# Performance work log

Measured on AMD Instinct MI355X. Metric: run time of the kernel, lower is better.

## Reference

```python
import jax, jax.numpy as jnp
import numpy as np

B = 4        # number of point clouds (equal-size contiguous batches)
P = 8192     # points per cloud
C_IN = 64
C_OUT = 64
K = 16       # kNN neighbors (includes the point itself, as in PyG knn)
EPS = 1e-5
NEG_SLOPE = 0.2


def setup_inputs() -> dict:
    key = jax.random.key(0)
    k1, k2, k3 = jax.random.split(key, 3)
    x = jax.random.normal(k1, (B * P, C_IN), dtype=jnp.float32)
    batch = jnp.repeat(jnp.arange(B, dtype=jnp.int64), P)  # sorted, equal sizes
    W = jax.random.normal(k2, (2 * C_IN, C_OUT), dtype=jnp.float32) * (1.0 / np.sqrt(2 * C_IN))
    b = jax.random.normal(k3, (C_OUT,), dtype=jnp.float32) * 0.01
    gamma = jnp.ones((C_OUT,), dtype=jnp.float32)
    beta = jnp.zeros((C_OUT,), dtype=jnp.float32)
    return {"x": x, "batch": batch, "W": W, "b": b, "gamma": gamma, "beta": beta}


def _edgeconv(x, W, b, gamma, beta):
    xb = x.reshape(B, P, C_IN)
    # per-cloud pairwise squared distances: [B, P, P]
    sq = jnp.sum(xb * xb, axis=-1)
    d = sq[:, :, None] + sq[:, None, :] - 2.0 * jnp.einsum("bpc,bqc->bpq", xb, xb)
    # k nearest neighbors (smallest distance, self included)
    _, idx = jax.lax.top_k(-d, K)                      # [B, P, K]
    xj = jax.vmap(lambda pts, ind: pts[ind])(xb, idx)  # [B, P, K, C_IN]
    xi = xb[:, :, None, :]
    e = jnp.concatenate([jnp.broadcast_to(xi, xj.shape), xj - xi], axis=-1)  # [B,P,K,2C]
    # edge MLP: Linear -> BatchNorm1d (training-mode batch stats over all edges) -> LeakyReLU
    h = jnp.einsum("bpke,eo->bpko", e, W) + b          # [B, P, K, C_OUT]
    hf = h.reshape(-1, C_OUT)
    mean = jnp.mean(hf, axis=0)
    var = jnp.mean(hf * hf, axis=0) - mean * mean      # biased variance (torch BN)
    hn = (h - mean) * jax.lax.rsqrt(var + EPS) * gamma + beta
    a = jnp.where(hn >= 0, hn, NEG_SLOPE * hn)
    # max aggregation over neighbors
    return jnp.max(a, axis=2).reshape(B * P, C_OUT)


def reference(x, batch, W, b, gamma, beta):
    # `batch` encodes B equal-size contiguous clouds; kNN is computed per cloud.
    return _edgeconv(x, W, b, gamma, beta)
```

## Files before the change

kernel.cpp:

```cpp
#include <hip/hip_runtime.h>
#include <cfloat>

#define BATCH 4
#define P 8192
#define C 64
#define KNN 16
#define NPTS (BATCH * P)
#define NEDGE (NPTS * KNN)
#define EPSV 1e-5f
#define SLOPE 0.2f
#define NQ 2
#define QCOLS (P / NQ)

typedef __attribute__((ext_vector_type(8))) short bf16x8;
typedef __attribute__((ext_vector_type(16))) float f32x16;


__device__ __forceinline__ unsigned short f2bf(float f) {
    unsigned u = __float_as_uint(f);
    u += 0x7FFFu + ((u >> 16) & 1u);
    return (unsigned short)(u >> 16);
}
__device__ __forceinline__ float bf2f(unsigned short s) {
    return __uint_as_float(((unsigned)s) << 16);
}

__global__ void prep_frag(const float* __restrict__ x, uint4* __restrict__ xfh,
                          uint4* __restrict__ xfm, uint4* __restrict__ xfl,
                          float* __restrict__ sq) {
    __shared__ float part[32][9];
    int tid = threadIdx.x;
    int ptl = tid >> 3, j8 = tid & 7;
    int g = blockIdx.x;
    int p = g * 32 + ptl;
    const float4* xp = (const float4*)(x + (size_t)p * C + j8 * 8);
    float4 a = xp[0], b = xp[1];
    float v[8] = {a.x, a.y, a.z, a.w, b.x, b.y, b.z, b.w};
    unsigned short hs[8], ms[8], ls[8];
    float ssum = 0.f;
#pragma unroll
    for (int e = 0; e < 8; ++e) {
        float xv = v[e];
        ssum = fmaf(xv, xv, ssum);
        unsigned short h = f2bf(xv);
        float r1 = xv - bf2f(h);
        unsigned short m = f2bf(r1);
        float r2 = r1 - bf2f(m);
        unsigned short l = f2bf(r2);
        hs[e] = h; ms[e] = m; ls[e] = l;
    }
    int dst = (g * 4 + (j8 >> 1)) * 64 + ptl + 32 * (j8 & 1);
    uint4 ph, pm, pl;
    ph.x = (unsigned)hs[0] | ((unsigned)hs[1] << 16);
    ph.y = (unsigned)hs[2] | ((unsigned)hs[3] << 16);
    ph.z = (unsigned)hs[4] | ((unsigned)hs[5] << 16);
    ph.w = (unsigned)hs[6] | ((unsigned)hs[7] << 16);
    pm.x = (unsigned)ms[0] | ((unsigned)ms[1] << 16);
    pm.y = (unsigned)ms[2] | ((unsigned)ms[3] << 16);
    pm.z = (unsigned)ms[4] | ((unsigned)ms[5] << 16);
    pm.w = (unsigned)ms[6] | ((unsigned)ms[7] << 16);
    pl.x = (unsigned)ls[0] | ((unsigned)ls[1] << 16);
    pl.y = (unsigned)ls[2] | ((unsigned)ls[3] << 16);
    pl.z = (unsigned)ls[4] | ((unsigned)ls[5] << 16);
    pl.w = (unsigned)ls[6] | ((unsigned)ls[7] << 16);
    xfh[dst] = ph; xfm[dst] = pm; xfl[dst] = pl;
    part[ptl][j8] = ssum;
    __syncthreads();
    if (j8 == 0) {
        float s = 0.f;
#pragma unroll
        for (int k = 0; k < 8; ++k) s += part[ptl][k];
        sq[p] = s;
    }
}

__global__ __launch_bounds__(256, 4) void knn_kernel(const uint4* __restrict__ xfh,
                                                     const uint4* __restrict__ xfm,
                                                     const uint4* __restrict__ xfl,
                                                     const float* __restrict__ sq,
                                                     float* __restrict__ pv,
                                                     int* __restrict__ pi) {
    __shared__ float bufv[64 * 65];
    __shared__ int   bufi[64 * 65];
    __shared__ int   idL[64 * 17];
    __shared__ int   cntL[64];
    __shared__ float worstL[64];

    int tid = threadIdx.x;
    int b = blockIdx.x & 3;
    int t = blockIdx.x >> 2;
    int tile = t & 127;
    int half = t >> 7;
    int bglob = b * P;
    int r0 = tile * 64;
    int colbase = half * QCOLS;
    int w = tid >> 6, lane = tid & 63;
    int wr = w & 1, wc = w >> 1;

    if (tid < 64) { cntL[tid] = 0; worstL[tid] = FLT_MAX; }

    int gA = ((bglob + r0) >> 5) + wr;
    bf16x8 Ah[4], Am[4], Al[4];
#pragma unroll
    for (int kk = 0; kk < 4; ++kk) {
        Ah[kk] = __builtin_bit_cast(bf16x8, xfh[(gA * 4 + kk) * 64 + lane]);
        Am[kk] = __builtin_bit_cast(bf16x8, xfm[(gA * 4 + kk) * 64 + lane]);
        Al[kk] = __builtin_bit_cast(bf16x8, xfl[(gA * 4 + kk) * 64 + lane]);
    }

    float tv[16];
    float worst = FLT_MAX;
#pragma unroll
    for (int j = 0; j < 16; ++j) tv[j] = FLT_MAX;
    int rown = w * 16 + (lane & 15);
    bool owner = (lane < 16);

    int rbase = wr * 32 + 4 * (lane >> 5);
    int colq = wc * 32 + (lane & 31);
    __syncthreads();

    for (int chunk = 0; chunk < QCOLS / 64; ++chunk) {
        int c0 = colbase + chunk * 64;
        int gB = ((bglob + c0) >> 5) + wc;
        bf16x8 Bh[4], Bm[4], Bl[4];
#pragma unroll
        for (int kk = 0; kk < 4; ++kk) {
            Bh[kk] = __builtin_bit_cast(bf16x8, xfh[(gB * 4 + kk) * 64 + lane]);
            Bm[kk] = __builtin_bit_cast(bf16x8, xfm[(gB * 4 + kk) * 64 + lane]);
            Bl[kk] = __builtin_bit_cast(bf16x8, xfl[(gB * 4 + kk) * 64 + lane]);
        }
        float sc = sq[bglob + c0 + colq];

        f32x16 acc0, acc1;
#pragma unroll
        for (int i = 0; i < 16; ++i) { acc0[i] = 0.f; acc1[i] = 0.f; }
#pragma unroll
        for (int kk = 0; kk < 4; ++kk) {
            acc0 = __builtin_amdgcn_mfma_f32_32x32x16_bf16(Ah[kk], Bh[kk], acc0, 0, 0, 0);
            acc1 = __builtin_amdgcn_mfma_f32_32x32x16_bf16(Ah[kk], Bm[kk], acc1, 0, 0, 0);
            acc0 = __builtin_amdgcn_mfma_f32_32x32x16_bf16(Am[kk], Bh[kk], acc0, 0, 0, 0);
            acc1 = __builtin_amdgcn_mfma_f32_32x32x16_bf16(Am[kk], Bm[kk], acc1, 0, 0, 0);
            acc0 = __builtin_amdgcn_mfma_f32_32x32x16_bf16(Ah[kk], Bl[kk], acc0, 0, 0, 0);
            acc1 = __builtin_amdgcn_mfma_f32_32x32x16_bf16(Al[kk], Bh[kk], acc1, 0, 0, 0);
        }

        if (chunk == 0) {
#pragma unroll
            for (int reg = 0; reg < 16; ++reg) {
                float s = fmaf(-2.f, acc0[reg] + acc1[reg], sc);
                int row = rbase + (reg & 3) + 8 * (reg >> 2);
                bufv[row * 65 + colq] = s;
            }
        } else {
            float4 twA[4];
#pragma unroll
            for (int g4 = 0; g4 < 4; ++g4)
                twA[g4] = *(const float4*)&worstL[rbase + 8 * g4];
            int colg = bglob + c0 + colq;
#pragma unroll
            for (int reg = 0; reg < 16; ++reg) {
                float s = fmaf(-2.f, acc0[reg] + acc1[reg], sc);
                float tW = ((const float*)&twA[reg >> 2])[reg & 3];
                if (s < tW) {
                    int row = rbase + (reg & 3) + 8 * (reg >> 2);
                    int slot = atomicAdd(&cntL[row], 1);
                    bufv[row * 65 + slot] = s;
                    bufi[row * 65 + slot] = colg;
                }
            }
        }
        __syncthreads();

        if (owner) {
            int n = (chunk == 0) ? 64 : cntL[rown];
            for (int k = 0; k < n; ++k) {
                float s = bufv[rown * 65 + k];
                if (s < worst) {
                    float mx = tv[0];
                    int pos = 0;
#pragma unroll
                    for (int j = 1; j < 16; ++j) {
                        bool g = tv[j] > mx;
                        mx = g ? tv[j] : mx;
                        pos = g ? j : pos;
                    }
#pragma unroll
                    for (int j = 0; j < 16; ++j)
                        if (j == pos) tv[j] = s;
                    idL[rown * 17 + pos] = (chunk == 0) ? (bglob + colbase + k)
                                                        : bufi[rown * 65 + k];
                    float nw = fmaxf(fmaxf(fmaxf(tv[0], tv[1]), fmaxf(tv[2], tv[3])),
                                     fmaxf(fmaxf(tv[4], tv[5]), fmaxf(tv[6], tv[7])));
                    nw = fmaxf(nw, fmaxf(fmaxf(fmaxf(tv[8], tv[9]), fmaxf(tv[10], tv[11])),
                                         fmaxf(fmaxf(tv[12], tv[13]), fmaxf(tv[14], tv[15]))));
                    worst = nw;
                }
            }
            cntL[rown] = 0;
            worstL[rown] = worst;
        }
        __syncthreads();
    }

    if (owner) {
        size_t o = (((size_t)(bglob + r0 + rown)) * NQ + half) * KNN;
#pragma unroll
        for (int j = 0; j < 16; ++j) {
            pv[o + j] = tv[j];
            pi[o + j] = idL[rown * 17 + j];
        }
    }
}

__global__ void merge_kernel(const float* __restrict__ pv, const int* __restrict__ pi,
                             int* __restrict__ idx_out) {
    __shared__ float mv[128 * 33];
    __shared__ int   mi[128 * 33];
    int tid = threadIdx.x;
    int lr = tid & 127, q = tid >> 7;
    int row = blockIdx.x * 128 + lr;
    size_t o = ((size_t)row * NQ + q) * KNN;
#pragma unroll
    for (int j = 0; j < 16; ++j) {
        mv[lr * 33 + q * 16 + j] = pv[o + j];
        mi[lr * 33 + q * 16 + j] = pi[o + j];
    }
    __syncthreads();
    if (tid < 128) {
        float tv[16];
        int ti[16];
        float worst = FLT_MAX;
#pragma unroll
        for (int j = 0; j < 16; ++j) { tv[j] = FLT_MAX; ti[j] = 0; }
        for (int e = 0; e < 32; ++e) {
            float s = mv[tid * 33 + e];
            if (s < worst) {
                float mx = tv[0];
                int pos = 0;
#pragma unroll
                for (int j = 1; j < 16; ++j) {
                    bool g = tv[j] > mx;
                    mx = g ? tv[j] : mx;
                    pos = g ? j : pos;
                }
#pragma unroll
                for (int j = 0; j < 16; ++j)
                    if (j == pos) { tv[j] = s; ti[j] = mi[tid * 33 + e]; }
                float nw = tv[0];
#pragma unroll
                for (int j = 1; j < 16; ++j) nw = fmaxf(nw, tv[j]);
                worst = nw;
            }
        }
        size_t oo = (size_t)row * KNN;
#pragma unroll
        for (int j = 0; j < 16; ++j) idx_out[oo + j] = ti[j];
    }
}

__global__ void prep_UV(const float* __restrict__ x, const float* __restrict__ W,
                        float* __restrict__ U, float* __restrict__ V) {
    __shared__ float Ws[128][64];
    __shared__ float xs[4][64];
    int tid = threadIdx.x;
    for (int i = tid; i < 128 * 64; i += 256) ((float*)Ws)[i] = W[i];
    int p0 = blockIdx.x * 4;
    int r = tid >> 6, c = tid & 63;
    xs[r][c] = x[(size_t)(p0 + r) * C + c];
    __syncthreads();
    float u = 0.f, v = 0.f;
#pragma unroll
    for (int k = 0; k < 64; ++k) {
        float xv = xs[r][k];
        float w1 = Ws[k][c];
        float w2 = Ws[64 + k][c];
        u = fmaf(xv, w1 - w2, u);
        v = fmaf(xv, w2, v);
    }
    size_t o = (size_t)(p0 + r) * C + c;
    U[o] = u;
    V[o] = v;
}

__global__ void stats_kernel(const float* __restrict__ U, const float* __restrict__ V,
                             const float* __restrict__ bias, const int* __restrict__ idx,
                             float* __restrict__ stats) {
    int tid = threadIdx.x;
    int c = tid & 63, kk = tid >> 6;
    int p0 = blockIdx.x * 32;
    float bc = bias[c];
    float sum = 0.f, sumsq = 0.f;
    for (int pp = 0; pp < 32; ++pp) {
        int p = p0 + pp;
        float u = U[(size_t)p * C + c] + bc;
#pragma unroll
        for (int k4 = 0; k4 < 4; ++k4) {
            int j = idx[(size_t)p * KNN + kk * 4 + k4];
            float h = u + V[(size_t)j * C + c];
            sum += h;
            sumsq = fmaf(h, h, sumsq);
        }
    }
    __shared__ float red[2][4][64];
    red[0][kk][c] = sum;
    red[1][kk][c] = sumsq;
    __syncthreads();
    if (tid < 64) {
        float s = red[0][0][tid] + red[0][1][tid] + red[0][2][tid] + red[0][3][tid];
        atomicAdd(&stats[tid], s);
    } else if (tid < 128) {
        int cc = tid - 64;
        float s = red[1][0][cc] + red[1][1][cc] + red[1][2][cc] + red[1][3][cc];
        atomicAdd(&stats[64 + cc], s);
    }
}

__global__ void finalize_kernel(const float* __restrict__ stats,
                                const float* __restrict__ gamma,
                                const float* __restrict__ beta,
                                float* __restrict__ sshift) {
    int c = threadIdx.x;
    const float N = (float)NEDGE;
    float mean = stats[c] / N;
    float var = stats[64 + c] / N - mean * mean;
    float s = gamma[c] * rsqrtf(var + EPSV);
    sshift[c] = s;
    sshift[64 + c] = beta[c] - mean * s;
}

__global__ void out_kernel(const float* __restrict__ U, const float* __restrict__ V,
                           const float* __restrict__ bias, const int* __restrict__ idx,
                           const float* __restrict__ sshift, float* __restrict__ out) {
    int tid = threadIdx.x;
    int c = tid & 63, g = tid >> 6;
    int p0 = blockIdx.x * 16;
    float s = sshift[c], t = sshift[64 + c];
    float bc = bias[c];
    for (int pp = g; pp < 16; pp += 4) {
        int p = p0 + pp;
        float mx = -FLT_MAX, mn = FLT_MAX;
#pragma unroll
        for (int k = 0; k < KNN; ++k) {
            int j = idx[(size_t)p * KNN + k];
            float v = V[(size_t)j * C + c];
            mx = fmaxf(mx, v);
            mn = fminf(mn, v);
        }
        float hsel = (s >= 0.f) ? mx : mn;
        float hn = fmaf(s, U[(size_t)p * C + c] + bc + hsel, t);
        out[(size_t)p * C + c] = (hn >= 0.f) ? hn : SLOPE * hn;
    }
}

extern "C" void kernel_launch(void* const* d_in, const int* in_sizes, int n_in,
                              void* d_out, int out_size, void* d_ws, size_t ws_size,
                              hipStream_t stream) {
    const float* x     = (const float*)d_in[0];
    const float* W     = (const float*)d_in[2];
    const float* bias  = (const float*)d_in[3];
    const float* gamma = (const float*)d_in[4];
    const float* beta  = (const float*)d_in[5];
    float* out = (float*)d_out;

    float* wsf    = (float*)d_ws;
    float* U      = wsf;
    float* V      = wsf + 2097152;
    uint4* xfh    = (uint4*)wsf;
    uint4* xfm    = (uint4*)(wsf + 1048576);
    uint4* xfl    = (uint4*)(wsf + 2097152);
    float* sq     = wsf + 4194304;
    float* stats  = wsf + 4227072;
    float* sshift = wsf + 4227200;
    int*   idx    = (int*)(wsf + 4227328);
    float* pv     = wsf + 4751616;
    int*   pi     = (int*)(wsf + 5800192);

    hipLaunchKernelGGL(prep_frag, dim3(NPTS / 32), dim3(256), 0, stream, x, xfh, xfm, xfl, sq);
    hipLaunchKernelGGL(knn_kernel, dim3(BATCH * (P / 64) * NQ), dim3(256), 0, stream,
                       (const uint4*)xfh, (const uint4*)xfm, (const uint4*)xfl, sq, pv, pi);
    hipLaunchKernelGGL(merge_kernel, dim3(NPTS / 128), dim3(256), 0, stream, pv, pi, idx);
    hipLaunchKernelGGL(prep_UV, dim3(NPTS / 4), dim3(256), 0, stream, x, W, U, V);
    hipMemsetAsync(stats, 0, 128 * sizeof(float), stream);
    hipLaunchKernelGGL(stats_kernel, dim3(NPTS / 32), dim3(256), 0, stream, U, V, bias, idx, stats);
    hipLaunchKernelGGL(finalize_kernel, dim3(1), dim3(64), 0, stream, stats, gamma, beta, sshift);
    hipLaunchKernelGGL(out_kernel, dim3(NPTS / 16), dim3(256), 0, stream, U, V, bias, idx, sshift, out);
}
```

Baseline: 574.8 us.

## Distribute kNN top-k across 16-lane groups and pipeline selection with next chunk's MFMA

Instead of one owner lane per row keeping a 16-entry register list (only 16 of 64 lanes active), each 16-lane group now holds one row's top-16 with one entry per lane, using ballot and shuffle-max reductions to replace the worst entry. Candidate buffers are double-buffered so selection for the previous chunk runs after the current chunk's MFMA, removing one barrier per chunk. The first three chunks are dense-scanned from a shared pool to seed thresholds. Per-row candidates are capped at 32 per chunk, which can drop true neighbors if more than 32 pass the threshold, and each insert now costs cross-lane shuffles.

```diff
diff --git a/kernel.cpp b/kernel.cpp
--- a/kernel.cpp
+++ b/kernel.cpp
@@ -11,6 +11,8 @@
 #define SLOPE 0.2f
 #define NQ 2
 #define QCOLS (P / NQ)
+#define NCH (QCOLS / 64)
+#define CAP 32
 
 typedef __attribute__((ext_vector_type(8))) short bf16x8;
 typedef __attribute__((ext_vector_type(16))) float f32x16;
@@ -80,11 +82,14 @@
                                                      const float* __restrict__ sq,
                                                      float* __restrict__ pv,
                                                      int* __restrict__ pi) {
-    __shared__ float bufv[64 * 65];
-    __shared__ int   bufi[64 * 65];
-    __shared__ int   idL[64 * 17];
-    __shared__ int   cntL[64];
+    __shared__ float bufv0[64 * CAP];
+    __shared__ int   bufi0[64 * CAP];
+    __shared__ float r1pool[64 * 68];
     __shared__ float worstL[64];
+    __shared__ int   cntA[2][64];
+
+    float* buf1v = r1pool;
+    int*   buf1i = (int*)(r1pool + 64 * CAP);
 
     int tid = threadIdx.x;
     int b = blockIdx.x & 3;
@@ -96,8 +101,11 @@
     int colbase = half * QCOLS;
     int w = tid >> 6, lane = tid & 63;
     int wr = w & 1, wc = w >> 1;
-
-    if (tid < 64) { cntL[tid] = 0; worstL[tid] = FLT_MAX; }
+    int g = lane >> 4, gl = lane & 15;
+    unsigned long long gmask = 0xFFFFull << (g * 16);
+    int myrow0 = w * 16 + g * 4;
+
+    if (tid < 128) ((int*)cntA)[tid] = 0;
 
     int gA = ((bglob + r0) >> 5) + wr;
     bf16x8 Ah[4], Am[4], Al[4];
@@ -108,18 +116,16 @@
         Al[kk] = __builtin_bit_cast(bf16x8, xfl[(gA * 4 + kk) * 64 + lane]);
     }
 
-    float tv[16];
-    float worst = FLT_MAX;
-#pragma unroll
-    for (int j = 0; j < 16; ++j) tv[j] = FLT_MAX;
-    int rown = w * 16 + (lane & 15);
-    bool owner = (lane < 16);
+    float tvq[4], wq[4];
+    int tiq[4];
+#pragma unroll
+    for (int rr = 0; rr < 4; ++rr) { tvq[rr] = FLT_MAX; wq[rr] = FLT_MAX; tiq[rr] = 0; }
 
     int rbase = wr * 32 + 4 * (lane >> 5);
     int colq = wc * 32 + (lane & 31);
     __syncthreads();
 
-    for (int chunk = 0; chunk < QCOLS / 64; ++chunk) {
+    for (int chunk = 0; chunk < NCH; ++chunk) {
         int c0 = colbase + chunk * 64;
         int gB = ((bglob + c0) >> 5) + wc;
         bf16x8 Bh[4], Bm[4], Bl[4];
@@ -144,14 +150,79 @@
             acc1 = __builtin_amdgcn_mfma_f32_32x32x16_bf16(Al[kk], Bh[kk], acc1, 0, 0, 0);
         }
 
-        if (chunk == 0) {
+        if (chunk >= 1) {
+            if (chunk <= 3) {
+                int idbase0 = bglob + colbase + (chunk - 1) * 64;
+#pragma unroll
+                for (int rr = 0; rr < 4; ++rr) {
+                    int row = myrow0 + rr;
+                    float tv = tvq[rr], worst = wq[rr];
+                    int ti = tiq[rr];
+                    const float* bv = &r1pool[row * 68];
+                    for (int k4 = 0; k4 < 64; k4 += 4) {
+                        float4 s4 = *(const float4*)(bv + k4);
+#pragma unroll
+                        for (int e = 0; e < 4; ++e) {
+                            float s = (e == 0) ? s4.x : (e == 1) ? s4.y : (e == 2) ? s4.z : s4.w;
+                            if (s < worst) {
+                                unsigned long long m = __ballot(tv == worst) & gmask;
+                                if (lane == (int)__builtin_ctzll(m)) { tv = s; ti = idbase0 + k4 + e; }
+                                float mx = tv;
+                                mx = fmaxf(mx, __shfl_xor(mx, 1));
+                                mx = fmaxf(mx, __shfl_xor(mx, 2));
+                                mx = fmaxf(mx, __shfl_xor(mx, 4));
+                                mx = fmaxf(mx, __shfl_xor(mx, 8));
+                                worst = mx;
+                            }
+                        }
+                    }
+                    tvq[rr] = tv; tiq[rr] = ti; wq[rr] = worst;
+                    if (gl == 0) worstL[row] = worst;
+                }
+            } else {
+                int mb = chunk & 1;
+                const float* mv = mb ? buf1v : bufv0;
+                const int*   mi = mb ? buf1i : bufi0;
+#pragma unroll
+                for (int rr = 0; rr < 4; ++rr) {
+                    int row = myrow0 + rr;
+                    float tv = tvq[rr], worst = wq[rr];
+                    int ti = tiq[rr];
+                    int n = cntA[mb][row]; n = (n > CAP) ? CAP : n;
+                    const float* bv = mv + row * CAP;
+                    const int*   bi = mi + row * CAP;
+                    for (int k = 0; k < n; ++k) {
+                        float s = bv[k];
+                        if (s < worst) {
+                            unsigned long long m = __ballot(tv == worst) & gmask;
+                            if (lane == (int)__builtin_ctzll(m)) { tv = s; ti = bi[k]; }
+                            float mx = tv;
+                            mx = fmaxf(mx, __shfl_xor(mx, 1));
+                            mx = fmaxf(mx, __shfl_xor(mx, 2));
+                            mx = fmaxf(mx, __shfl_xor(mx, 4));
+                            mx = fmaxf(mx, __shfl_xor(mx, 8));
+                            worst = mx;
+                        }
+                    }
+                    tvq[rr] = tv; tiq[rr] = ti; wq[rr] = worst;
+                    if (gl == 0) worstL[row] = worst;
+                    if (gl == 1) cntA[mb][row] = 0;
+                }
+            }
+            __syncthreads();
+        }
+
+        if (chunk <= 2) {
 #pragma unroll
             for (int reg = 0; reg < 16; ++reg) {
                 float s = fmaf(-2.f, acc0[reg] + acc1[reg], sc);
                 int row = rbase + (reg & 3) + 8 * (reg >> 2);
-                bufv[row * 65 + colq] = s;
+                r1pool[row * 68 + colq] = s;
             }
         } else {
+            int ab = (chunk - 3) & 1;
+            float* av = ab ? buf1v : bufv0;
+            int*   ai = ab ? buf1i : bufi0;
             float4 twA[4];
 #pragma unroll
             for (int g4 = 0; g4 < 4; ++g4)
@@ -163,52 +234,49 @@
                 float tW = ((const float*)&twA[reg >> 2])[reg & 3];
                 if (s < tW) {
                     int row = rbase + (reg & 3) + 8 * (reg >> 2);
-                    int slot = atomicAdd(&cntL[row], 1);
-                    bufv[row * 65 + slot] = s;
-                    bufi[row * 65 + slot] = colg;
+                    int slot = atomicAdd(&cntA[ab][row], 1);
+                    if (slot < CAP) { av[row * CAP + slot] = s; ai[row * CAP + slot] = colg; }
                 }
             }
         }
         __syncthreads();
-
-        if (owner) {
-            int n = (chunk == 0) ? 64 : cntL[rown];
+    }
+
+    {
+        int mb = NCH & 1;
+        const float* mv = mb ? buf1v : bufv0;
+        const int*   mi = mb ? buf1i : bufi0;
+#pragma unroll
+        for (int rr = 0; rr < 4; ++rr) {
+            int row = myrow0 + rr;
+            float tv = tvq[rr], worst = wq[rr];
+            int ti = tiq[rr];
+            int n = cntA[mb][row]; n = (n > CAP) ? CAP : n;
+            const float* bv = mv + row * CAP;
+            const int*   bi = mi + row * CAP;
             for (int k = 0; k < n; ++k) {
-                float s = bufv[rown * 65 + k];
+                float s = bv[k];
                 if (s < worst) {
-                    float mx = tv[0];
-                    int pos = 0;
-#pragma unroll
-                    for (int j = 1; j < 16; ++j) {
-                        bool g = tv[j] > mx;
-                        mx = g ? tv[j] : mx;
-                        pos = g ? j : pos;
-                    }
-#pragma unroll
-                    for (int j = 0; j < 16; ++j)
-                        if (j == pos) tv[j] = s;
-                    idL[rown * 17 + pos] = (chunk == 0) ? (bglob + colbase + k)
-                                                        : bufi[rown * 65 + k];
-                    float nw = fmaxf(fmaxf(fmaxf(tv[0], tv[1]), fmaxf(tv[2], tv[3])),
-                                     fmaxf(fmaxf(tv[4], tv[5]), fmaxf(tv[6], tv[7])));
-                    nw = fmaxf(nw, fmaxf(fmaxf(fmaxf(tv[8], tv[9]), fmaxf(tv[10], tv[11])),
-                                         fmaxf(fmaxf(tv[12], tv[13]), fmaxf(tv[14], tv[15]))));
-                    worst = nw;
+                    unsigned long long m = __ballot(tv == worst) & gmask;
+                    if (lane == (int)__builtin_ctzll(m)) { tv = s; ti = bi[k]; }
+                    float mx = tv;
+                    mx = fmaxf(mx, __shfl_xor(mx, 1));
+                    mx = fmaxf(mx, __shfl_xor(mx, 2));
+                    mx = fmaxf(mx, __shfl_xor(mx, 4));
+                    mx = fmaxf(mx, __shfl_xor(mx, 8));
+                    worst = mx;
                 }
             }
-            cntL[rown] = 0;
-            worstL[rown] = worst;
-        }
-        __syncthreads();
-    }
-
-    if (owner) {
-        size_t o = (((size_t)(bglob + r0 + rown)) * NQ + half) * KNN;
-#pragma unroll
-        for (int j = 0; j < 16; ++j) {
-            pv[o + j] = tv[j];
-            pi[o + j] = idL[rown * 17 + j];
-        }
+            tvq[rr] = tv; tiq[rr] = ti;
+        }
+    }
+
+#pragma unroll
+    for (int rr = 0; rr < 4; ++rr) {
+        int row = myrow0 + rr;
+        size_t o = (((size_t)(bglob + r0 + row)) * NQ + half) * KNN;
+        pv[o + gl] = tvq[rr];
+        pi[o + gl] = tiq[rr];
     }
 }
 
```

Result: slower. 697.5 us (+21.3%).

## Batch kNN candidate merges on power-of-two chunks using packed keys and rank sort

Applied to the files above, without the earlier changes.

Distances and indices are packed into monotonic 64-bit keys, so each row keeps a single top-16 key array. The per-chunk serial insertion by one owner lane is replaced with a wave-parallel rank-based merge. That merge runs only after chunks 0, 1, 3, 7 and so on, which removes most block-wide barriers and most merge work. The cost is that candidates are filtered against a stale threshold between merges. They go into a fixed 52-slot buffer, so a row that overflows it silently drops candidates and could return wrong neighbors.

```diff
diff --git a/kernel.cpp b/kernel.cpp
--- a/kernel.cpp
+++ b/kernel.cpp
@@ -11,6 +11,8 @@
 #define SLOPE 0.2f
 #define NQ 2
 #define QCOLS (P / NQ)
+#define NCH (QCOLS / 64)
+#define CAP 52
 
 typedef __attribute__((ext_vector_type(8))) short bf16x8;
 typedef __attribute__((ext_vector_type(16))) float f32x16;
@@ -23,6 +25,14 @@
 }
 __device__ __forceinline__ float bf2f(unsigned short s) {
     return __uint_as_float(((unsigned)s) << 16);
+}
+__device__ __forceinline__ unsigned monof(float f) {
+    unsigned u = __float_as_uint(f);
+    return u ^ ((unsigned)((int)u >> 31) | 0x80000000u);
+}
+__device__ __forceinline__ float invmonof(unsigned k) {
+    unsigned u = (k & 0x80000000u) ? (k ^ 0x80000000u) : ~k;
+    return __uint_as_float(u);
 }
 
 __global__ void prep_frag(const float* __restrict__ x, uint4* __restrict__ xfh,
@@ -80,11 +90,10 @@
                                                      const float* __restrict__ sq,
                                                      float* __restrict__ pv,
                                                      int* __restrict__ pi) {
-    __shared__ float bufv[64 * 65];
-    __shared__ int   bufi[64 * 65];
-    __shared__ int   idL[64 * 17];
-    __shared__ int   cntL[64];
+    __shared__ unsigned long long bufk[64 * CAP];
+    __shared__ unsigned long long topk[64 * 16];
     __shared__ float worstL[64];
+    __shared__ int   cnt[64];
 
     int tid = threadIdx.x;
     int b = blockIdx.x & 3;
@@ -97,7 +106,7 @@
     int w = tid >> 6, lane = tid & 63;
     int wr = w & 1, wc = w >> 1;
 
-    if (tid < 64) { cntL[tid] = 0; worstL[tid] = FLT_MAX; }
+    if (tid < 64) cnt[tid] = 0;
 
     int gA = ((bglob + r0) >> 5) + wr;
     bf16x8 Ah[4], Am[4], Al[4];
@@ -108,18 +117,10 @@
         Al[kk] = __builtin_bit_cast(bf16x8, xfl[(gA * 4 + kk) * 64 + lane]);
     }
 
-    float tv[16];
-    float worst = FLT_MAX;
-#pragma unroll
-    for (int j = 0; j < 16; ++j) tv[j] = FLT_MAX;
-    int rown = w * 16 + (lane & 15);
-    bool owner = (lane < 16);
-
     int rbase = wr * 32 + 4 * (lane >> 5);
     int colq = wc * 32 + (lane & 31);
-    __syncthreads();
-
-    for (int chunk = 0; chunk < QCOLS / 64; ++chunk) {
+
+    for (int chunk = 0; chunk < NCH; ++chunk) {
         int c0 = colbase + chunk * 64;
         int gB = ((bglob + c0) >> 5) + wc;
         bf16x8 Bh[4], Bm[4], Bl[4];
@@ -144,70 +145,66 @@
             acc1 = __builtin_amdgcn_mfma_f32_32x32x16_bf16(Al[kk], Bh[kk], acc1, 0, 0, 0);
         }
 
+        int colg = bglob + c0 + colq;
         if (chunk == 0) {
 #pragma unroll
             for (int reg = 0; reg < 16; ++reg) {
                 float s = fmaf(-2.f, acc0[reg] + acc1[reg], sc);
                 int row = rbase + (reg & 3) + 8 * (reg >> 2);
-                bufv[row * 65 + colq] = s;
+                unsigned long long key =
+                    ((unsigned long long)monof(s) << 32) | (unsigned)colg;
+                if (colq < 16) topk[row * 16 + colq] = key;
+                else           bufk[row * CAP + (colq - 16)] = key;
             }
         } else {
             float4 twA[4];
 #pragma unroll
             for (int g4 = 0; g4 < 4; ++g4)
                 twA[g4] = *(const float4*)&worstL[rbase + 8 * g4];
-            int colg = bglob + c0 + colq;
 #pragma unroll
             for (int reg = 0; reg < 16; ++reg) {
                 float s = fmaf(-2.f, acc0[reg] + acc1[reg], sc);
                 float tW = ((const float*)&twA[reg >> 2])[reg & 3];
                 if (s < tW) {
                     int row = rbase + (reg & 3) + 8 * (reg >> 2);
-                    int slot = atomicAdd(&cntL[row], 1);
-                    bufv[row * 65 + slot] = s;
-                    bufi[row * 65 + slot] = colg;
+                    int slot = atomicAdd(&cnt[row], 1);
+                    if (slot < CAP)
+                        bufk[row * CAP + slot] =
+                            ((unsigned long long)monof(s) << 32) | (unsigned)colg;
                 }
             }
         }
-        __syncthreads();
-
-        if (owner) {
-            int n = (chunk == 0) ? 64 : cntL[rown];
-            for (int k = 0; k < n; ++k) {
-                float s = bufv[rown * 65 + k];
-                if (s < worst) {
-                    float mx = tv[0];
-                    int pos = 0;
-#pragma unroll
-                    for (int j = 1; j < 16; ++j) {
-                        bool g = tv[j] > mx;
-                        mx = g ? tv[j] : mx;
-                        pos = g ? j : pos;
-                    }
-#pragma unroll
-                    for (int j = 0; j < 16; ++j)
-                        if (j == pos) tv[j] = s;
-                    idL[rown * 17 + pos] = (chunk == 0) ? (bglob + colbase + k)
-                                                        : bufi[rown * 65 + k];
-                    float nw = fmaxf(fmaxf(fmaxf(tv[0], tv[1]), fmaxf(tv[2], tv[3])),
-                                     fmaxf(fmaxf(tv[4], tv[5]), fmaxf(tv[6], tv[7])));
-                    nw = fmaxf(nw, fmaxf(fmaxf(fmaxf(tv[8], tv[9]), fmaxf(tv[10], tv[11])),
-                                         fmaxf(fmaxf(tv[12], tv[13]), fmaxf(tv[14], tv[15]))));
-                    worst = nw;
-                }
+
+        if ((chunk & (chunk + 1)) == 0) {
+            __syncthreads();
+            for (int rr = 0; rr < 16; ++rr) {
+                int row = w * 16 + rr;
+                int n = (chunk == 0) ? 48 : (cnt[row] < CAP ? cnt[row] : CAP);
+                unsigned long long mykey;
+                if (lane < 16)            mykey = topk[row * 16 + lane];
+                else if (lane < 16 + n)   mykey = bufk[row * CAP + (lane - 16)];
+                else                      mykey = ~0ull;
+                int rank = 0;
+#pragma unroll
+                for (int j = 0; j < 16; ++j)
+                    rank += (topk[row * 16 + j] < mykey) ? 1 : 0;
+                for (int j = 0; j < n; ++j)
+                    rank += (bufk[row * CAP + j] < mykey) ? 1 : 0;
+                if (rank < 16) topk[row * 16 + rank] = mykey;
+                if (rank == 15) worstL[row] = invmonof((unsigned)(mykey >> 32));
+                if (lane == 0) cnt[row] = 0;
             }
-            cntL[rown] = 0;
-            worstL[rown] = worst;
-        }
-        __syncthreads();
-    }
-
-    if (owner) {
-        size_t o = (((size_t)(bglob + r0 + rown)) * NQ + half) * KNN;
-#pragma unroll
-        for (int j = 0; j < 16; ++j) {
-            pv[o + j] = tv[j];
-            pi[o + j] = idL[rown * 17 + j];
+            __syncthreads();
+        }
+    }
+
+    for (int rr = 0; rr < 16; ++rr) {
+        int row = w * 16 + rr;
+        if (lane < 16) {
+            unsigned long long k = topk[row * 16 + lane];
+            size_t o = (((size_t)(bglob + r0 + row)) * NQ + half) * KNN;
+            pv[o + lane] = invmonof((unsigned)(k >> 32));
+            pi[o + lane] = (int)(unsigned)(k & 0xFFFFFFFFu);
         }
     }
 }
```

Result: slower. 599.2 us (+4.2%).
